# Optimization experiments

Measured on AMD Instinct MI355X. Metric: run time of the kernel, lower is better.

The kernel has to match this reference:

```python
import jax, jax.numpy as jnp
import numpy as np

B, S, E = 4, 1024, 768
H, HD = 8, 96  # heads, head_dim (E = H*HD)


def setup_inputs() -> dict:
    key = jax.random.key(0)
    ks = jax.random.split(key, 32)
    init = lambda k, shape: jax.random.normal(k, shape, jnp.float32) * 0.02
    d = {
        'sequence_features': jax.random.normal(ks[0], (B, S, E), jnp.float32),
        # backbone_network: Linear(E,E) ReLU Dropout Linear(E,E)
        'bb_w1': init(ks[1], (E, E)), 'bb_b1': init(ks[2], (E,)),
        'bb_w2': init(ks[3], (E, E)), 'bb_b2': init(ks[4], (E,)),
        # side_chain_network: Linear(E,E//2) ReLU Dropout Linear(E//2,E)
        'sc_w1': init(ks[5], (E, E // 2)), 'sc_b1': init(ks[6], (E // 2,)),
        'sc_w2': init(ks[7], (E // 2, E)), 'sc_b2': init(ks[8], (E,)),
        # contact predictor: MultiheadAttention(E, 8) + MLP(E->384->1)
        'attn_wq': init(ks[9], (E, E)), 'attn_bq': init(ks[10], (E,)),
        'attn_wk': init(ks[11], (E, E)), 'attn_bk': init(ks[12], (E,)),
        'attn_wv': init(ks[13], (E, E)), 'attn_bv': init(ks[14], (E,)),
        'attn_wo': init(ks[15], (E, E)), 'attn_bo': init(ks[16], (E,)),
        'mlp_w1': init(ks[17], (E, 384)), 'mlp_b1': init(ks[18], (384,)),
        'mlp_w2': init(ks[19], (384, 1)), 'mlp_b2': init(ks[20], (1,)),
        # structure refiner processors
        'rb_w1': init(ks[21], (E, 384)), 'rb_b1': init(ks[22], (384,)),
        'rb_w2': init(ks[23], (384, 3)), 'rb_b2': init(ks[24], (3,)),
        'rs_w1': init(ks[25], (E, 384)), 'rs_b1': init(ks[26], (384,)),
        'rs_w2': init(ks[27], (384, 4)), 'rs_b2': init(ks[28], (4,)),
    }
    return d


def _pdist(s):
    # batched pairwise euclidean distances with torch-cdist-like zero-grad at d=0
    xx = jnp.sum(s * s, axis=-1)
    d2 = xx[:, :, None] + xx[:, None, :] - 2.0 * jnp.einsum('bid,bjd->bij', s, s)
    d2 = jnp.maximum(d2, 0.0)
    safe = jnp.sqrt(jnp.where(d2 > 0, d2, 1.0))
    return jnp.where(d2 > 0, safe, 0.0)


def reference(sequence_features, bb_w1, bb_b1, bb_w2, bb_b2, sc_w1, sc_b1, sc_w2, sc_b2,
              attn_wq, attn_bq, attn_wk, attn_bk, attn_wv, attn_bv, attn_wo, attn_bo,
              mlp_w1, mlp_b1, mlp_w2, mlp_b2, rb_w1, rb_b1, rb_w2, rb_b2,
              rs_w1, rs_b1, rs_w2, rs_b2):
    x = sequence_features  # [B,S,E]
    # backbone / side-chain feature networks (dropout = identity at eval)
    backbone = jax.nn.relu(x @ bb_w1 + bb_b1) @ bb_w2 + bb_b2            # [B,S,E]
    side = jax.nn.relu(backbone @ sc_w1 + sc_b1) @ sc_w2 + sc_b2        # [B,S,E]

    # --- ContactMapPredictor ---
    # torch MHA default batch_first=False: input [B,S,E] is treated as (L=B, N=S, E),
    # i.e. attention runs OVER THE BATCH AXIS. Faithfully reproduced.
    q = (x @ attn_wq + attn_bq).reshape(B, S, H, HD)
    k = (x @ attn_wk + attn_bk).reshape(B, S, H, HD)
    v = (x @ attn_wv + attn_bv).reshape(B, S, H, HD)
    scores = jnp.einsum('bshd,cshd->shbc', q, k) / jnp.sqrt(jnp.float32(HD))
    attn = jax.nn.softmax(scores, axis=-1)
    ao = jnp.einsum('shbc,cshd->bshd', attn, v).reshape(B, S, E) @ attn_wo + attn_bo
    probs = jax.nn.relu(ao @ mlp_w1 + mlp_b1) @ mlp_w2 + mlp_b2          # [B,S,1]
    # contacts[:, i, :] = probs[:, i] broadcast over last axis
    contacts = jnp.broadcast_to(probs, (B, S, S))

    # --- StructureRefiner ---
    ba = jax.nn.relu(backbone @ rb_w1 + rb_b1) @ rb_w2 + rb_b2           # [B,S,3]
    sa = jax.nn.relu(side @ rs_w1 + rs_b1) @ rs_w2 + rs_b2               # [B,S,4], computed but unused (as in source)
    del sa
    phi, psi = ba[..., 0], ba[..., 1]  # omega unused in source
    steps = 3.8 * jnp.stack([jnp.cos(phi) * jnp.cos(psi),
                             jnp.sin(phi) * jnp.cos(psi),
                             jnp.sin(psi)], axis=-1)                      # [B,S,3]
    steps = steps.at[:, 0].set(0.0)  # structure[:,0] stays at origin
    structure = jnp.cumsum(steps, axis=1)  # the serial i-loop is a cumsum

    def loss_fn(s):
        dists = _pdist(s)
        contact_loss = jnp.mean(jnp.abs(dists - 8.0) * contacts)
        diag = jnp.diagonal(dists, axis1=1, axis2=2)
        chain_loss = jnp.mean(jnp.abs(diag - 3.8))
        return contact_loss + chain_loss

    lr, beta1, beta2, eps = 0.01, 0.9, 0.999, 1e-8

    def adam_step(carry, t):
        s, m, v = carry
        g = jax.grad(loss_fn)(s)
        m = beta1 * m + (1.0 - beta1) * g
        v = beta2 * v + (1.0 - beta2) * g * g
        mhat = m / (1.0 - beta1 ** t)
        vhat = v / (1.0 - beta2 ** t)
        s = s - lr * mhat / (jnp.sqrt(vhat) + eps)
        return (s, m, v), None

    ts = jnp.arange(1, 51, dtype=jnp.float32)
    (structure, _, _), _ = jax.lax.scan(
        adam_step, (structure, jnp.zeros_like(structure), jnp.zeros_like(structure)), ts)
    structure = jax.lax.stop_gradient(structure)  # .detach() in source

    return backbone, side, contacts, structure
```

## Files before the change

kernel.cpp:

```cpp
#include <hip/hip_runtime.h>
#include <cmath>

static constexpr int Bb = 4, Ss = 1024, Ee = 768, Hh = 8, HDd = 96;
static constexpr int BS = Bb * Ss;
static constexpr size_t SLOT_EF = (size_t)BS * Ee;

typedef __attribute__((ext_vector_type(8))) short short8v;
typedef __attribute__((ext_vector_type(4))) float f32x4;

__device__ __forceinline__ ushort f2b(float f) {
    unsigned u = __float_as_uint(f);
    return (ushort)((u + 0x7FFFu + ((u >> 16) & 1u)) >> 16);
}
__device__ __forceinline__ float b2f(ushort b) {
    return __uint_as_float(((unsigned)b) << 16);
}
__device__ __forceinline__ void gload16(const void* g, void* l) {
    __builtin_amdgcn_global_load_lds(
        (const __attribute__((address_space(1))) unsigned int*)g,
        (__attribute__((address_space(3))) unsigned int*)l, 16, 0, 0);
}

__global__ __launch_bounds__(256) void cvt_bf16_k(
    const float* __restrict__ in, ushort* __restrict__ out, int n)
{
    const int i = (blockIdx.x * 256 + threadIdx.x) * 4;
    if (i >= n) return;
    const float4 v = *reinterpret_cast<const float4*>(in + i);
    ushort4 o;
    o.x = f2b(v.x); o.y = f2b(v.y); o.z = f2b(v.z); o.w = f2b(v.w);
    *reinterpret_cast<ushort4*>(out + i) = o;
}

struct TDesc { const float* src; ushort* dst; int K; int N; int tile0; };
struct TPack { TDesc e[10]; };

__global__ __launch_bounds__(256) void tcvt_multi_k(TPack p)
{
    __shared__ float tile[64][65];
    const int tb = blockIdx.x;
    int idx = 0;
#pragma unroll
    for (int i = 1; i < 10; ++i) if (tb >= p.e[i].tile0) idx = i;
    const TDesc d = p.e[idx];
    const int lt = tb - d.tile0;
    const int ntn = d.N >> 6;
    const int nb = (lt % ntn) << 6;
    const int kb = (lt / ntn) << 6;
    const int t = threadIdx.x;
    {
        const int nn = t & 63, k4 = t >> 6;
#pragma unroll
        for (int r = 0; r < 16; ++r) {
            const int kk = (k4 << 4) + r;
            tile[kk][nn] = d.src[(size_t)(kb + kk) * d.N + nb + nn];
        }
    }
    __syncthreads();
    {
        const int kk = t & 63, n4 = t >> 6;
#pragma unroll
        for (int r = 0; r < 16; ++r) {
            const int nn = (n4 << 4) + r;
            d.dst[(size_t)(nb + nn) * d.K + kb + kk] = f2b(tile[kk][nn]);
        }
    }
}

__global__ __launch_bounds__(256) void concat_bias_k(
    const float* __restrict__ a, const float* __restrict__ b,
    const float* __restrict__ c, float* __restrict__ o)
{
    const int i = blockIdx.x * 256 + threadIdx.x;
    if (i < 768) o[i] = a[i];
    else if (i < 1536) o[i] = b[i - 768];
    else if (i < 2304) o[i] = c[i - 1536];
}

template <int RELU, int WF32, int WB16>
__global__ __launch_bounds__(256) void gemm_bf16_k(
    const ushort* __restrict__ A, const ushort* __restrict__ Bt,
    const float* __restrict__ bias,
    float* __restrict__ Cf, ushort* __restrict__ Cb,
    int M, int N, int K)
{
    __shared__ ushort As[128 * 32];
    __shared__ ushort Bs[128 * 32];
    const int t = threadIdx.x, lane = t & 63, wid = t >> 6;
    const int bm = blockIdx.y, bn = blockIdx.x;
    const int wr = wid >> 1, wc = wid & 1;

    const int r0 = wid * 32 + (lane >> 2);
    const int sc = (lane & 3) * 8;
    const ushort* Ag0 = A  + (size_t)(bm * 128 + r0) * K + sc;
    const ushort* Ag1 = Ag0 + (size_t)16 * K;
    const ushort* Bg0 = Bt + (size_t)(bn * 128 + r0) * K + sc;
    const ushort* Bg1 = Bg0 + (size_t)16 * K;
    char* AsB = (char*)As + wid * 2048;
    char* BsB = (char*)Bs + wid * 2048;

    f32x4 acc[4][4];
#pragma unroll
    for (int m = 0; m < 4; ++m)
#pragma unroll
        for (int n = 0; n < 4; ++n) acc[m][n] = (f32x4){0.f, 0.f, 0.f, 0.f};

    const int fr = lane & 15, ks = (lane >> 4) * 8;

    for (int k0 = 0; k0 < K; k0 += 32) {
        __syncthreads();
        gload16(Ag0 + k0, AsB);
        gload16(Ag1 + k0, AsB + 1024);
        gload16(Bg0 + k0, BsB);
        gload16(Bg1 + k0, BsB + 1024);
        __syncthreads();

        short8v a[4], b[4];
#pragma unroll
        for (int m = 0; m < 4; ++m)
            a[m] = *reinterpret_cast<const short8v*>(&As[(wr * 64 + m * 16 + fr) * 32 + ks]);
#pragma unroll
        for (int n = 0; n < 4; ++n)
            b[n] = *reinterpret_cast<const short8v*>(&Bs[(wc * 64 + n * 16 + fr) * 32 + ks]);
#pragma unroll
        for (int m = 0; m < 4; ++m)
#pragma unroll
            for (int n = 0; n < 4; ++n)
                acc[m][n] = __builtin_amdgcn_mfma_f32_16x16x32_bf16(a[m], b[n], acc[m][n], 0, 0, 0);
    }

    const int col0 = bn * 128 + wc * 64 + (lane & 15);
    const int rw0  = bm * 128 + wr * 64 + (lane >> 4) * 4;
#pragma unroll
    for (int n = 0; n < 4; ++n) {
        const int col = col0 + n * 16;
        const float bv = bias[col];
#pragma unroll
        for (int m = 0; m < 4; ++m) {
            const f32x4 v = acc[m][n];
#pragma unroll
            for (int r = 0; r < 4; ++r) {
                const int row = rw0 + m * 16 + r;
                float val = v[r] + bv;
                if (RELU) val = fmaxf(val, 0.f);
                if (WF32) Cf[(size_t)row * N + col] = val;
                if (WB16) Cb[(size_t)row * N + col] = f2b(val);
            }
        }
    }
}

__global__ __launch_bounds__(256) void attn_wave_k(
    const ushort* __restrict__ qkv, ushort* __restrict__ ao)
{
    const int wv = (blockIdx.x << 2) + (threadIdx.x >> 6);
    const int lane = threadIdx.x & 63;
    const int s = wv >> 3, h = wv & 7;
    const int c0 = h * HDd;
    const bool has2 = lane < 32;

    float qq[4][2], kk[4][2];
#pragma unroll
    for (int b = 0; b < 4; ++b) {
        const size_t base = (size_t)(b * Ss + s) * 2304 + c0;
        qq[b][0] = b2f(qkv[base + lane]);
        qq[b][1] = has2 ? b2f(qkv[base + 64 + lane]) : 0.f;
        kk[b][0] = b2f(qkv[base + 768 + lane]);
        kk[b][1] = has2 ? b2f(qkv[base + 768 + 64 + lane]) : 0.f;
    }
    float sc[4][4];
#pragma unroll
    for (int b = 0; b < 4; ++b)
#pragma unroll
        for (int c = 0; c < 4; ++c)
            sc[b][c] = qq[b][0] * kk[c][0] + qq[b][1] * kk[c][1];
#pragma unroll
    for (int msk = 1; msk < 64; msk <<= 1)
#pragma unroll
        for (int b = 0; b < 4; ++b)
#pragma unroll
            for (int c = 0; c < 4; ++c)
                sc[b][c] += __shfl_xor(sc[b][c], msk, 64);

    const float scale = 0.10206207261596577f;
    float at[4][4];
#pragma unroll
    for (int b = 0; b < 4; ++b) {
        const float mx = fmaxf(fmaxf(sc[b][0], sc[b][1]), fmaxf(sc[b][2], sc[b][3]));
        float sum = 0.f;
#pragma unroll
        for (int c = 0; c < 4; ++c) { at[b][c] = expf((sc[b][c] - mx) * scale); sum += at[b][c]; }
        const float inv = 1.f / sum;
#pragma unroll
        for (int c = 0; c < 4; ++c) at[b][c] *= inv;
    }

    float vv[4][2];
#pragma unroll
    for (int c = 0; c < 4; ++c) {
        const size_t base = (size_t)(c * Ss + s) * 2304 + 1536 + c0;
        vv[c][0] = b2f(qkv[base + lane]);
        vv[c][1] = has2 ? b2f(qkv[base + 64 + lane]) : 0.f;
    }
#pragma unroll
    for (int b = 0; b < 4; ++b) {
        float o0 = 0.f, o1 = 0.f;
#pragma unroll
        for (int c = 0; c < 4; ++c) { o0 = fmaf(at[b][c], vv[c][0], o0); o1 = fmaf(at[b][c], vv[c][1], o1); }
        const size_t obase = (size_t)(b * Ss + s) * Ee + c0;
        ao[obase + lane] = f2b(o0);
        if (has2) ao[obase + 64 + lane] = f2b(o1);
    }
}

__global__ __launch_bounds__(256) void mlp2_probs_k(
    const float* __restrict__ m1, const float* __restrict__ w2,
    const float* __restrict__ b2, float* __restrict__ probs)
{
    const int gid = blockIdx.x * 256 + threadIdx.x;
    const int row = gid >> 6, lane = gid & 63;
    if (row >= BS) return;
    float acc = 0.f;
    for (int kk = lane; kk < 384; kk += 64)
        acc = fmaf(m1[(size_t)row * 384 + kk], w2[kk], acc);
#pragma unroll
    for (int off = 32; off > 0; off >>= 1) acc += __shfl_down(acc, off, 64);
    if (lane == 0) probs[row] = acc + b2[0];
}

__global__ __launch_bounds__(256) void rb2_ba_k(
    const float* __restrict__ r1, const float* __restrict__ w2,
    const float* __restrict__ b2, float* __restrict__ ba)
{
    const int gid = blockIdx.x * 256 + threadIdx.x;
    const int row = gid >> 6, lane = gid & 63;
    if (row >= BS) return;
    float a0 = 0.f, a1 = 0.f, a2 = 0.f;
    for (int kk = lane; kk < 384; kk += 64) {
        const float r = r1[(size_t)row * 384 + kk];
        a0 = fmaf(r, w2[kk * 3 + 0], a0);
        a1 = fmaf(r, w2[kk * 3 + 1], a1);
        a2 = fmaf(r, w2[kk * 3 + 2], a2);
    }
#pragma unroll
    for (int off = 32; off > 0; off >>= 1) {
        a0 += __shfl_down(a0, off, 64);
        a1 += __shfl_down(a1, off, 64);
        a2 += __shfl_down(a2, off, 64);
    }
    if (lane == 0) {
        ba[(size_t)row * 3 + 0] = a0 + b2[0];
        ba[(size_t)row * 3 + 1] = a1 + b2[1];
        ba[(size_t)row * 3 + 2] = a2 + b2[2];
    }
}

__global__ __launch_bounds__(256) void contacts_k(
    const float* __restrict__ probs, float* __restrict__ out)
{
    const int f4 = blockIdx.x * 256 + threadIdx.x;
    if (f4 >= (Bb * Ss * Ss) / 4) return;
    const int row = f4 >> 8;
    const float p = probs[row];
    reinterpret_cast<float4*>(out)[f4] = make_float4(p, p, p, p);
}

__global__ __launch_bounds__(1024) void steps_cumsum_k(
    const float* __restrict__ ba, float* __restrict__ sPad)
{
    const int b = blockIdx.x;
    const int i = threadIdx.x;
    const int row = b * Ss + i;
    const float phi = ba[(size_t)row * 3 + 0];
    const float psi = ba[(size_t)row * 3 + 1];
    const float cpsi = cosf(psi);
    float x = 3.8f * cosf(phi) * cpsi;
    float y = 3.8f * sinf(phi) * cpsi;
    float z = 3.8f * sinf(psi);
    if (i == 0) { x = 0.f; y = 0.f; z = 0.f; }
    __shared__ float sx[1024], sy[1024], sz[1024];
    sx[i] = x; sy[i] = y; sz[i] = z;
    for (int off = 1; off < 1024; off <<= 1) {
        __syncthreads();
        float ax = 0.f, ay = 0.f, az = 0.f;
        if (i >= off) { ax = sx[i - off]; ay = sy[i - off]; az = sz[i - off]; }
        __syncthreads();
        sx[i] += ax; sy[i] += ay; sz[i] += az;
    }
    *reinterpret_cast<float4*>(sPad + ((size_t)row << 2)) = make_float4(sx[i], sy[i], sz[i], 0.f);
}

__global__ __launch_bounds__(512) void adam_coop4_k(
    float* __restrict__ sA, float* __restrict__ sB, float* __restrict__ outS,
    const float* __restrict__ probs, unsigned* flags)
{
    const int tid = threadIdx.x, lane = tid & 63, wv = tid >> 6;
    const int bk = blockIdx.x;
    const int batch = bk >> 6;
    const int jbase = batch << 10;
    const int lr = (bk & 63) * 16 + wv * 2;
    const int rbase = jbase + lr;

    __shared__ float sx[1024], sy[1024], sz[1024], pSh[1024];
    for (int i = tid; i < 1024; i += 512) pSh[i] = probs[jbase + i];

    float m[2][3] = {}, v[2][3] = {};
    float pb1 = 1.f, pb2 = 1.f;
    const float invN = 1.f / 4194304.f;

    for (int t = 1; t <= 50; ++t) {
        const float* rbuf = (t & 1) ? sA : sB;
        float* wbuf = (t & 1) ? sB : sA;
        for (int r = tid; r < 1024; r += 512) {
            const float4 q = *reinterpret_cast<const float4*>(rbuf + (((size_t)(jbase + r)) << 2));
            sx[r] = q.x; sy[r] = q.y; sz[r] = q.z;
        }
        __syncthreads();

        pb1 *= 0.9f; pb2 *= 0.999f;
        const float bc1 = 1.f / (1.f - pb1);
        const float bc2 = 1.f / (1.f - pb2);

        float srx[2], sry[2], srz[2], pr[2], g[2][3] = {};
#pragma unroll
        for (int r = 0; r < 2; ++r) {
            srx[r] = sx[lr + r]; sry[r] = sy[lr + r]; srz[r] = sz[lr + r]; pr[r] = pSh[lr + r];
        }

        for (int it = 0; it < 16; ++it) {
            const int j = it * 64 + lane;
            const float qx = sx[j], qy = sy[j], qz = sz[j];
            const float pj = pSh[j];
#pragma unroll
            for (int r = 0; r < 2; ++r) {
                const float dx = srx[r] - qx, dy = sry[r] - qy, dz = srz[r] - qz;
                const float d2 = dx * dx + dy * dy + dz * dz;
                if (d2 > 0.f) {
                    const float w = ((d2 > 64.f) ? 1.f : -1.f) * (pr[r] + pj) * rsqrtf(d2);
                    g[r][0] = fmaf(w, dx, g[r][0]);
                    g[r][1] = fmaf(w, dy, g[r][1]);
                    g[r][2] = fmaf(w, dz, g[r][2]);
                }
            }
        }
#pragma unroll
        for (int msk = 1; msk < 64; msk <<= 1)
#pragma unroll
            for (int r = 0; r < 2; ++r)
#pragma unroll
                for (int c = 0; c < 3; ++c)
                    g[r][c] += __shfl_xor(g[r][c], msk, 64);

        float ns[2][3];
#pragma unroll
        for (int r = 0; r < 2; ++r) {
            const float sc_[3] = { srx[r], sry[r], srz[r] };
#pragma unroll
            for (int c = 0; c < 3; ++c) {
                const float gg = g[r][c] * invN;
                m[r][c] = 0.9f * m[r][c] + 0.1f * gg;
                v[r][c] = 0.999f * v[r][c] + 0.001f * gg * gg;
                ns[r][c] = sc_[c] - 0.01f * (m[r][c] * bc1) / (sqrtf(v[r][c] * bc2) + 1e-8f);
            }
        }

        if (t == 50) {
            if (lane == 0) {
#pragma unroll
                for (int r = 0; r < 2; ++r)
#pragma unroll
                    for (int c = 0; c < 3; ++c)
                        outS[(size_t)(rbase + r) * 3 + c] = ns[r][c];
            }
            return;
        }

        if (lane == 0) {
#pragma unroll
            for (int r = 0; r < 2; ++r) {
                float* dst = wbuf + (((size_t)(rbase + r)) << 2);
                const unsigned long long xy =
                    ((unsigned long long)__float_as_uint(ns[r][1]) << 32)
                    | (unsigned long long)__float_as_uint(ns[r][0]);
                __hip_atomic_store((unsigned long long*)dst, xy,
                                   __ATOMIC_RELAXED, __HIP_MEMORY_SCOPE_AGENT);
                __hip_atomic_store(dst + 2, ns[r][2],
                                   __ATOMIC_RELAXED, __HIP_MEMORY_SCOPE_AGENT);
            }
        }
        __syncthreads();
        if (tid == 0)
            __hip_atomic_store(&flags[bk * 32], (unsigned)t,
                               __ATOMIC_RELEASE, __HIP_MEMORY_SCOPE_AGENT);
        if (tid < 64) {
            while (__hip_atomic_load(&flags[((batch << 6) + tid) * 32], __ATOMIC_RELAXED,
                                     __HIP_MEMORY_SCOPE_AGENT) < (unsigned)t)
                __builtin_amdgcn_s_sleep(2);
            __builtin_amdgcn_fence(__ATOMIC_ACQUIRE, "agent");
        }
        __syncthreads();
    }
}

extern "C" void kernel_launch(void* const* d_in, const int* in_sizes, int n_in,
                              void* d_out, int out_size, void* d_ws, size_t ws_size,
                              hipStream_t stream)
{
    const float* x     = (const float*)d_in[0];
    const float* bb_w1 = (const float*)d_in[1];
    const float* bb_b1 = (const float*)d_in[2];
    const float* bb_w2 = (const float*)d_in[3];
    const float* bb_b2 = (const float*)d_in[4];
    const float* sc_w1 = (const float*)d_in[5];
    const float* sc_b1 = (const float*)d_in[6];
    const float* sc_w2 = (const float*)d_in[7];
    const float* sc_b2 = (const float*)d_in[8];
    const float* wq_p = (const float*)d_in[9];  const float* bq = (const float*)d_in[10];
    const float* wk_p = (const float*)d_in[11]; const float* bk = (const float*)d_in[12];
    const float* wv_p = (const float*)d_in[13]; const float* bv = (const float*)d_in[14];
    const float* wo_p = (const float*)d_in[15]; const float* bo = (const float*)d_in[16];
    const float* mlp_w1 = (const float*)d_in[17]; const float* mlp_b1 = (const float*)d_in[18];
    const float* mlp_w2 = (const float*)d_in[19]; const float* mlp_b2 = (const float*)d_in[20];
    const float* rb_w1 = (const float*)d_in[21]; const float* rb_b1 = (const float*)d_in[22];
    const float* rb_w2 = (const float*)d_in[23]; const float* rb_b2 = (const float*)d_in[24];

    float* out_backbone = (float*)d_out;
    float* out_side     = out_backbone + SLOT_EF;
    float* out_contacts = out_side + SLOT_EF;
    float* out_struct   = out_contacts + (size_t)Bb * Ss * Ss;

    ushort* cur = (ushort*)d_ws;
    ushort* xb        = cur; cur += SLOT_EF;
    ushort* mb        = cur; cur += SLOT_EF;
    ushort* backboneb = cur; cur += SLOT_EF;
    ushort* s1b       = cur; cur += (size_t)BS * 384;
    ushort* bb_w1t    = cur; cur += 768 * 768;
    ushort* bb_w2t    = cur; cur += 768 * 768;
    ushort* qkvWt     = cur; cur += 2304 * 768;
    ushort* wot       = cur; cur += 768 * 768;
    ushort* sc_w1t    = cur; cur += 768 * 384;
    ushort* sc_w2t    = cur; cur += 768 * 384;
    ushort* mlp_w1t   = cur; cur += 768 * 384;
    ushort* rb_w1t    = cur; cur += 768 * 384;
    float* fcur = (float*)cur;
    float* qkvBias = fcur; fcur += 2304;
    float* probs   = fcur; fcur += BS;
    float* ba      = fcur; fcur += 3 * BS;
    float* sPA     = fcur; fcur += 4 * BS;
    float* sPB     = fcur; fcur += 4 * BS;
    unsigned* flags = (unsigned*)fcur; fcur += 256 * 32;

    ushort* qkvb = (ushort*)out_backbone;
    ushort* aob  = (ushort*)out_contacts;
    ushort* h1b  = (ushort*)out_contacts;
    float*  m1f  = out_side + (size_t)BS * 384;
    float*  r1f  = (float*)xb;

    const dim3 blk(256);
    const dim3 gEE(768 / 128, BS / 128);
    const dim3 gEH(384 / 128, BS / 128);
    const dim3 gQKV(2304 / 128, BS / 128);

    cvt_bf16_k<<<dim3((int)(SLOT_EF / 4 / 256)), blk, 0, stream>>>(x, xb, (int)SLOT_EF);
    {
        TPack tp; int t0 = 0; int ti = 0;
        auto add = [&](const float* s, ushort* d, int K, int N) {
            tp.e[ti].src = s; tp.e[ti].dst = d; tp.e[ti].K = K; tp.e[ti].N = N; tp.e[ti].tile0 = t0;
            t0 += (N / 64) * (K / 64); ++ti;
        };
        add(bb_w1, bb_w1t, 768, 768);
        add(bb_w2, bb_w2t, 768, 768);
        add(wq_p, qkvWt,                 768, 768);
        add(wk_p, qkvWt + 768 * 768,     768, 768);
        add(wv_p, qkvWt + 2 * 768 * 768, 768, 768);
        add(wo_p, wot, 768, 768);
        add(sc_w1, sc_w1t, 768, 384);
        add(sc_w2, sc_w2t, 384, 768);
        add(mlp_w1, mlp_w1t, 768, 384);
        add(rb_w1, rb_w1t, 768, 384);
        tcvt_multi_k<<<dim3(t0), blk, 0, stream>>>(tp);
    }
    concat_bias_k<<<dim3(9), blk, 0, stream>>>(bq, bk, bv, qkvBias);

    gemm_bf16_k<0, 0, 1><<<gQKV, blk, 0, stream>>>(xb, qkvWt, qkvBias, nullptr, qkvb, BS, 2304, 768);
    attn_wave_k<<<dim3(Ss * Hh / 4), blk, 0, stream>>>(qkvb, aob);
    gemm_bf16_k<0, 0, 1><<<gEE, blk, 0, stream>>>(aob, wot, bo, nullptr, mb, BS, 768, 768);
    gemm_bf16_k<1, 1, 0><<<gEH, blk, 0, stream>>>(mb, mlp_w1t, mlp_b1, m1f, nullptr, BS, 384, 768);
    mlp2_probs_k<<<dim3(BS * 64 / 256), blk, 0, stream>>>(m1f, mlp_w2, mlp_b2, probs);

    gemm_bf16_k<1, 0, 1><<<gEE, blk, 0, stream>>>(xb, bb_w1t, bb_b1, nullptr, h1b, BS, 768, 768);
    gemm_bf16_k<0, 1, 1><<<gEE, blk, 0, stream>>>(h1b, bb_w2t, bb_b2, out_backbone, backboneb, BS, 768, 768);
    gemm_bf16_k<1, 0, 1><<<gEH, blk, 0, stream>>>(backboneb, sc_w1t, sc_b1, nullptr, s1b, BS, 384, 768);
    gemm_bf16_k<0, 1, 0><<<gEE, blk, 0, stream>>>(s1b, sc_w2t, sc_b2, out_side, nullptr, BS, 768, 384);

    contacts_k<<<dim3(Bb * Ss * Ss / 4 / 256), blk, 0, stream>>>(probs, out_contacts);

    gemm_bf16_k<1, 1, 0><<<gEH, blk, 0, stream>>>(backboneb, rb_w1t, rb_b1, r1f, nullptr, BS, 384, 768);
    rb2_ba_k<<<dim3(BS * 64 / 256), blk, 0, stream>>>(r1f, rb_w2, rb_b2, ba);
    steps_cumsum_k<<<dim3(Bb), dim3(1024), 0, stream>>>(ba, sPA);

    hipMemsetAsync(flags, 0, 256 * 32 * sizeof(unsigned), stream);
    {
        void* args[] = { (void*)&sPA, (void*)&sPB, (void*)&out_struct, (void*)&probs,
                         (void*)&flags };
        hipLaunchCooperativeKernel(reinterpret_cast<void*>(adam_coop4_k),
                                   dim3(256), dim3(512), args, 0, stream);
    }
}
```

Measured before the change: 694.0 us.

## Replace cooperative flag-synced Adam loop with 50 per-step kernel launches

The single cooperative kernel, which synchronised blocks through global flag spinning between Adam iterations, is replaced by 50 separate launches of a one-step kernel. The Adam moments m and v move from registers into a global buffer that each step reads and writes. The bias-correction factors are now computed on the host in double precision. This removes the spin-wait barrier and the cooperative launch, at the cost of 50 launch overheads plus the extra global traffic for the moments and for reloading probs each step.

```diff
diff --git a/kernel.cpp b/kernel.cpp
--- a/kernel.cpp
+++ b/kernel.cpp
@@ -290,9 +290,10 @@
     *reinterpret_cast<float4*>(sPad + ((size_t)row << 2)) = make_float4(sx[i], sy[i], sz[i], 0.f);
 }
 
-__global__ __launch_bounds__(512) void adam_coop4_k(
-    float* __restrict__ sA, float* __restrict__ sB, float* __restrict__ outS,
-    const float* __restrict__ probs, unsigned* flags)
+__global__ __launch_bounds__(512) void adam_step2_k(
+    const float* __restrict__ sIn, float* __restrict__ sOut,
+    float* __restrict__ mv, const float* __restrict__ probs,
+    float* __restrict__ outS, float bc1, float bc2, int last)
 {
     const int tid = threadIdx.x, lane = tid & 63, wv = tid >> 6;
     const int bk = blockIdx.x;
@@ -303,102 +304,73 @@
 
     __shared__ float sx[1024], sy[1024], sz[1024], pSh[1024];
     for (int i = tid; i < 1024; i += 512) pSh[i] = probs[jbase + i];
-
-    float m[2][3] = {}, v[2][3] = {};
-    float pb1 = 1.f, pb2 = 1.f;
+    for (int r = tid; r < 1024; r += 512) {
+        const float4 q = *reinterpret_cast<const float4*>(sIn + (((size_t)(jbase + r)) << 2));
+        sx[r] = q.x; sy[r] = q.y; sz[r] = q.z;
+    }
+    __syncthreads();
+
     const float invN = 1.f / 4194304.f;
-
-    for (int t = 1; t <= 50; ++t) {
-        const float* rbuf = (t & 1) ? sA : sB;
-        float* wbuf = (t & 1) ? sB : sA;
-        for (int r = tid; r < 1024; r += 512) {
-            const float4 q = *reinterpret_cast<const float4*>(rbuf + (((size_t)(jbase + r)) << 2));
-            sx[r] = q.x; sy[r] = q.y; sz[r] = q.z;
-        }
-        __syncthreads();
-
-        pb1 *= 0.9f; pb2 *= 0.999f;
-        const float bc1 = 1.f / (1.f - pb1);
-        const float bc2 = 1.f / (1.f - pb2);
-
-        float srx[2], sry[2], srz[2], pr[2], g[2][3] = {};
+    float srx[2], sry[2], srz[2], pr[2], g[2][3] = {};
+#pragma unroll
+    for (int r = 0; r < 2; ++r) {
+        srx[r] = sx[lr + r]; sry[r] = sy[lr + r]; srz[r] = sz[lr + r]; pr[r] = pSh[lr + r];
+    }
+
+    for (int it = 0; it < 16; ++it) {
+        const int j = it * 64 + lane;
+        const float qx = sx[j], qy = sy[j], qz = sz[j];
+        const float pj = pSh[j];
 #pragma unroll
         for (int r = 0; r < 2; ++r) {
-            srx[r] = sx[lr + r]; sry[r] = sy[lr + r]; srz[r] = sz[lr + r]; pr[r] = pSh[lr + r];
-        }
-
-        for (int it = 0; it < 16; ++it) {
-            const int j = it * 64 + lane;
-            const float qx = sx[j], qy = sy[j], qz = sz[j];
-            const float pj = pSh[j];
-#pragma unroll
-            for (int r = 0; r < 2; ++r) {
-                const float dx = srx[r] - qx, dy = sry[r] - qy, dz = srz[r] - qz;
-                const float d2 = dx * dx + dy * dy + dz * dz;
-                if (d2 > 0.f) {
-                    const float w = ((d2 > 64.f) ? 1.f : -1.f) * (pr[r] + pj) * rsqrtf(d2);
-                    g[r][0] = fmaf(w, dx, g[r][0]);
-                    g[r][1] = fmaf(w, dy, g[r][1]);
-                    g[r][2] = fmaf(w, dz, g[r][2]);
-                }
+            const float dx = srx[r] - qx, dy = sry[r] - qy, dz = srz[r] - qz;
+            const float d2 = dx * dx + dy * dy + dz * dz;
+            if (d2 > 0.f) {
+                const float w = ((d2 > 64.f) ? 1.f : -1.f) * (pr[r] + pj) * rsqrtf(d2);
+                g[r][0] = fmaf(w, dx, g[r][0]);
+                g[r][1] = fmaf(w, dy, g[r][1]);
+                g[r][2] = fmaf(w, dz, g[r][2]);
             }
         }
-#pragma unroll
-        for (int msk = 1; msk < 64; msk <<= 1)
-#pragma unroll
-            for (int r = 0; r < 2; ++r)
-#pragma unroll
-                for (int c = 0; c < 3; ++c)
-                    g[r][c] += __shfl_xor(g[r][c], msk, 64);
-
-        float ns[2][3];
+    }
+#pragma unroll
+    for (int msk = 1; msk < 64; msk <<= 1)
+#pragma unroll
+        for (int r = 0; r < 2; ++r)
+#pragma unroll
+            for (int c = 0; c < 3; ++c)
+                g[r][c] += __shfl_xor(g[r][c], msk, 64);
+
+    if (lane == 0) {
 #pragma unroll
         for (int r = 0; r < 2; ++r) {
+            const int row = rbase + r;
+            float4 mva = *reinterpret_cast<const float4*>(mv + ((size_t)row << 3));
+            float4 mvb = *reinterpret_cast<const float4*>(mv + ((size_t)row << 3) + 4);
+            float mArr[3] = { mva.x, mva.y, mva.z };
+            float vArr[3] = { mva.w, mvb.x, mvb.y };
             const float sc_[3] = { srx[r], sry[r], srz[r] };
+            float ns[3];
 #pragma unroll
             for (int c = 0; c < 3; ++c) {
                 const float gg = g[r][c] * invN;
-                m[r][c] = 0.9f * m[r][c] + 0.1f * gg;
-                v[r][c] = 0.999f * v[r][c] + 0.001f * gg * gg;
-                ns[r][c] = sc_[c] - 0.01f * (m[r][c] * bc1) / (sqrtf(v[r][c] * bc2) + 1e-8f);
+                mArr[c] = 0.9f * mArr[c] + 0.1f * gg;
+                vArr[c] = 0.999f * vArr[c] + 0.001f * gg * gg;
+                ns[c] = sc_[c] - 0.01f * (mArr[c] * bc1) / (sqrtf(vArr[c] * bc2) + 1e-8f);
+            }
+            *reinterpret_cast<float4*>(mv + ((size_t)row << 3)) =
+                make_float4(mArr[0], mArr[1], mArr[2], vArr[0]);
+            *reinterpret_cast<float4*>(mv + ((size_t)row << 3) + 4) =
+                make_float4(vArr[1], vArr[2], 0.f, 0.f);
+            if (last) {
+                outS[(size_t)row * 3 + 0] = ns[0];
+                outS[(size_t)row * 3 + 1] = ns[1];
+                outS[(size_t)row * 3 + 2] = ns[2];
+            } else {
+                *reinterpret_cast<float4*>(sOut + ((size_t)row << 2)) =
+                    make_float4(ns[0], ns[1], ns[2], 0.f);
             }
         }
-
-        if (t == 50) {
-            if (lane == 0) {
-#pragma unroll
-                for (int r = 0; r < 2; ++r)
-#pragma unroll
-                    for (int c = 0; c < 3; ++c)
-                        outS[(size_t)(rbase + r) * 3 + c] = ns[r][c];
-            }
-            return;
-        }
-
-        if (lane == 0) {
-#pragma unroll
-            for (int r = 0; r < 2; ++r) {
-                float* dst = wbuf + (((size_t)(rbase + r)) << 2);
-                const unsigned long long xy =
-                    ((unsigned long long)__float_as_uint(ns[r][1]) << 32)
-                    | (unsigned long long)__float_as_uint(ns[r][0]);
-                __hip_atomic_store((unsigned long long*)dst, xy,
-                                   __ATOMIC_RELAXED, __HIP_MEMORY_SCOPE_AGENT);
-                __hip_atomic_store(dst + 2, ns[r][2],
-                                   __ATOMIC_RELAXED, __HIP_MEMORY_SCOPE_AGENT);
-            }
-        }
-        __syncthreads();
-        if (tid == 0)
-            __hip_atomic_store(&flags[bk * 32], (unsigned)t,
-                               __ATOMIC_RELEASE, __HIP_MEMORY_SCOPE_AGENT);
-        if (tid < 64) {
-            while (__hip_atomic_load(&flags[((batch << 6) + tid) * 32], __ATOMIC_RELAXED,
-                                     __HIP_MEMORY_SCOPE_AGENT) < (unsigned)t)
-                __builtin_amdgcn_s_sleep(2);
-            __builtin_amdgcn_fence(__ATOMIC_ACQUIRE, "agent");
-        }
-        __syncthreads();
     }
 }
 
@@ -448,7 +420,7 @@
     float* ba      = fcur; fcur += 3 * BS;
     float* sPA     = fcur; fcur += 4 * BS;
     float* sPB     = fcur; fcur += 4 * BS;
-    unsigned* flags = (unsigned*)fcur; fcur += 256 * 32;
+    float* mvB     = fcur; fcur += 8 * BS;
 
     ushort* qkvb = (ushort*)out_backbone;
     ushort* aob  = (ushort*)out_contacts;
@@ -499,11 +471,13 @@
     rb2_ba_k<<<dim3(BS * 64 / 256), blk, 0, stream>>>(r1f, rb_w2, rb_b2, ba);
     steps_cumsum_k<<<dim3(Bb), dim3(1024), 0, stream>>>(ba, sPA);
 
-    hipMemsetAsync(flags, 0, 256 * 32 * sizeof(unsigned), stream);
-    {
-        void* args[] = { (void*)&sPA, (void*)&sPB, (void*)&out_struct, (void*)&probs,
-                         (void*)&flags };
-        hipLaunchCooperativeKernel(reinterpret_cast<void*>(adam_coop4_k),
-                                   dim3(256), dim3(512), args, 0, stream);
-    }
-}
+    hipMemsetAsync(mvB, 0, (size_t)8 * BS * sizeof(float), stream);
+    for (int t = 1; t <= 50; ++t) {
+        const float bc1 = (float)(1.0 / (1.0 - std::pow(0.9, (double)t)));
+        const float bc2 = (float)(1.0 / (1.0 - std::pow(0.999, (double)t)));
+        const float* sin_ = (t & 1) ? sPA : sPB;
+        float* sout = (t & 1) ? sPB : sPA;
+        adam_step2_k<<<dim3(256), dim3(512), 0, stream>>>(
+            sin_, sout, mvB, probs, out_struct, bc1, bc2, (t == 50) ? 1 : 0);
+    }
+}
```

Measured after the change: 613.3 us. 11.6% less time.
